# Optimization experiments

Measured on AMD Instinct MI355X. Metric: run time of the kernel, lower is better.

Reference implementation:

```python
import jax, jax.numpy as jnp
import numpy as np
from jax import lax

N = 200; E = 3200; HID = 64; NH = 16; OUT = 2 * HID; CAT = NH * OUT  # CAT = 2048
ALPHA = 0.2


def _gat(h, e_attr, adj, n2n, W, a_s, a_d, a_e, We, concat):
    # edge-feature-aware GAT head: logits from Wh_i, Wh_j and projected node2node feats
    Nn = h.shape[0]
    Wh = h @ W                                       # [N, out]
    ee = ((n2n @ We) @ a_e).reshape(Nn, Nn)          # [N, N] edge-feature term
    logits = jax.nn.leaky_relu((Wh @ a_s)[:, None] + (Wh @ a_d)[None, :] + ee,
                               negative_slope=ALPHA)
    logits = jnp.where(adj > 0, logits, -1e9)        # mask to graph structure
    att = jax.nn.softmax(logits, axis=1)
    h2 = att @ Wh
    if concat:
        h2 = jax.nn.elu(h2)
    return h2, jax.nn.elu(e_attr @ We)               # updated node + edge features


def _edge_pool(x, eidx, e, w, b):
    # static-shape edge pooling: score edges, gate nodes by mean incident score
    src, dst = eidx[0], eidx[1]
    s = jax.nn.sigmoid(jnp.concatenate([x[src], x[dst], e], axis=1) @ w + b)  # [E]
    deg = jax.ops.segment_sum(jnp.ones_like(s), src, num_segments=x.shape[0])
    ns = jax.ops.segment_sum(s, src, num_segments=x.shape[0]) / (deg + 1e-6)
    return x * ns[:, None], e * s[:, None]


def _gpool(x, w, b):
    # GlobalAttention: gate_nn = Linear+Sigmoid, softmax over nodes, weighted sum
    gate = jax.nn.softmax(jax.nn.sigmoid(x @ w + b), axis=0)  # [N, 1]
    return jnp.sum(gate * x, axis=0, keepdims=True)           # [1, D]


def _adj_n2n(Nn, eidx, eattr):
    # vectorized version of the per-edge Python loop in _get_adj_node2node
    src, dst = eidx[0], eidx[1]
    adj = jnp.zeros((Nn, Nn), eattr.dtype).at[src, dst].set(1.0)
    n2n = jnp.zeros((Nn * Nn, eattr.shape[1]), eattr.dtype).at[src * Nn + dst].set(eattr)
    return adj, n2n


def _lstm_dir(x, Wih, Whh, b):
    # one LSTM direction over seq x [T, Din] (PyTorch i,f,g,o gate order)
    Hh = Whh.shape[1]
    def step(carry, xt):
        h, c = carry
        g = xt @ Wih.T + h @ Whh.T + b
        i, f, gg, o = jnp.split(g, 4)
        c = jax.nn.sigmoid(f) * c + jax.nn.sigmoid(i) * jnp.tanh(gg)
        h = jax.nn.sigmoid(o) * jnp.tanh(c)
        return (h, c), h
    (_, _), ys = lax.scan(step, (jnp.zeros(Hh, x.dtype), jnp.zeros(Hh, x.dtype)), x)
    return ys


def setup_inputs():
    key = jax.random.key(0)
    ks = iter(jax.random.split(key, 64))
    def rn(shape, scale=0.05):
        return jax.random.normal(next(ks), shape, jnp.float32) * scale
    inp = {}
    for g in (1, 2):
        eidx = jax.random.randint(next(ks), (2, E), 0, N)
        eattr = rn((E, HID), 1.0)
        adj, n2n = _adj_n2n(N, eidx, eattr)
        inp['features%d' % g] = rn((N, HID), 1.0)
        inp['edge_index%d' % g] = eidx
        inp['edgesAttr%d' % g] = eattr
        inp['adjacency%d' % g] = adj
        inp['node2node%d' % g] = n2n
    inp.update(dict(
        W_h=rn((HID, HID)),
        W_gat=rn((NH, HID, OUT)), a_src=rn((NH, OUT)), a_dst=rn((NH, OUT)),
        a_e=rn((NH, OUT)), We_gat=rn((NH, HID, OUT)),
        W_out=rn((CAT, OUT)), ao_src=rn((OUT,)), ao_dst=rn((OUT,)), ao_e=rn((OUT,)),
        We_out=rn((CAT, OUT)),
        ep1_w=rn((3 * CAT,)), ep1_b=rn(()),
        ep2_w=rn((3 * OUT,)), ep2_b=rn(()),
        g1_w=rn((HID, 1)), g1_b=rn((1,)),
        g2_w=rn((CAT, 1)), g2_b=rn((1,)),
        g3_w=rn((OUT, 1)), g3_b=rn((1,)),
        Wih0=rn((2, 512, 35 * HID)), Whh0=rn((2, 512, 128)), b0=rn((2, 512)),
        Wih1=rn((2, 512, 256)), Whh1=rn((2, 512, 128)), b1=rn((2, 512)),
        fc_w=rn((256, 2)), fc_b=rn((2,)),
    ))
    return inp


def reference(features1, features2, edge_index1, edge_index2, edgesAttr1, edgesAttr2,
              adjacency1, adjacency2, node2node1, node2node2,
              W_h, W_gat, a_src, a_dst, a_e, We_gat,
              W_out, ao_src, ao_dst, ao_e, We_out,
              ep1_w, ep1_b, ep2_w, ep2_b,
              g1_w, g1_b, g2_w, g2_b, g3_w, g3_b,
              Wih0, Whh0, b0, Wih1, Whh1, b1, fc_w, fc_b):
    def graph(feat, eidx, eattr, adj, n2n):
        h = jax.nn.elu(feat @ W_h)                              # SingleNodeAttentionLayer
        hs = [_gpool(h, g1_w, g1_b)]
        outs = [_gat(h, eattr, adj, n2n, W_gat[i], a_src[i], a_dst[i], a_e[i],
                     We_gat[i], True) for i in range(NH)]
        h = jnp.concatenate([o[0] for o in outs], axis=1)       # [N, 2048]
        eattr = jnp.concatenate([o[1] for o in outs], axis=1)   # [E, 2048]
        h, eattr = _edge_pool(h, eidx, eattr, ep1_w, ep1_b)
        hs.append(_gpool(h, g2_w, g2_b))
        adj2, n2n2 = _adj_n2n(h.shape[0], eidx, eattr)          # dense [N*N, 2048]
        h, eattr = _gat(h, eattr, adj2, n2n2, W_out, ao_src, ao_dst, ao_e, We_out, False)
        h, eattr = _edge_pool(h, eidx, eattr, ep2_w, ep2_b)
        hs.append(_gpool(h, g3_w, g3_b))
        return jnp.concatenate(hs, axis=1)                      # [1, 35*HID]

    h1 = graph(features1, edge_index1, edgesAttr1, adjacency1, node2node1)
    h2 = graph(features2, edge_index2, edgesAttr2, adjacency2, node2node2)
    x = jnp.concatenate([h1, h2], axis=0)                       # seq [2, 2240]
    for Wih, Whh, b in ((Wih0, Whh0, b0), (Wih1, Whh1, b1)):
        f = _lstm_dir(x, Wih[0], Whh[0], b[0])
        r = _lstm_dir(x[::-1], Wih[1], Whh[1], b[1])[::-1]
        x = jnp.concatenate([f, r], axis=1)                     # [2, 256]
    logits = x[-1] @ fc_w + fc_b
    return jax.nn.softmax(logits)[None, :]                      # [1, nclass]
```

## Files before the change

kernel.cpp:

```cpp
#include <hip/hip_runtime.h>
#include <math.h>

#define DI static __device__ __forceinline__

DI float eluf(float x){ return x > 0.f ? x : expm1f(x); }
DI float lreluf(float x){ return x > 0.f ? x : 0.2f*x; }
DI float sigmf(float x){ return 1.f/(1.f+expf(-x)); }

typedef unsigned short u16;
typedef unsigned int   u32;
typedef __attribute__((ext_vector_type(8))) short short8_t;
typedef __attribute__((ext_vector_type(4))) float f32x4;

DI u16 bf16rne(float f){
  u32 u = __float_as_uint(f);
  u += 0x7fffu + ((u>>16)&1u);
  return (u16)(u>>16);
}

DI f32x4 bmfma(short8_t a, short8_t b, f32x4 c){
  return __builtin_amdgcn_mfma_f32_16x16x32_bf16(a, b, c, 0, 0, 0);
}

constexpr int N=200, E=3200, HID=64, NH=16, OUTD=128, CAT=2048, SEQD=2240;

constexpr int OH0   = 0;
constexpr int OWH   = OH0 + N*HID;
constexpr int OASN  = OWH + NH*N*OUTD;
constexpr int OADN  = OASN + NH*N;
constexpr int OH1   = OADN + NH*N;
constexpr int OXW1  = OH1 + N*CAT;
constexpr int OXW2  = OXW1 + 256;
constexpr int OEW1  = OXW2 + 256;
constexpr int OS1   = OEW1 + E;
constexpr int ODEG1 = OS1 + E;
constexpr int OSS1  = ODEG1 + 256;
constexpr int ORAW1 = OSS1 + 256;
constexpr int OWH2  = ORAW1 + 256;
constexpr int OAS2  = OWH2 + N*OUTD;
constexpr int OAD2  = OAS2 + 256;
constexpr int OEWV  = OAD2 + 256;
constexpr int OH2B  = OEWV + E;
constexpr int OXS2  = OH2B + N*OUTD;
constexpr int OXD2  = OXS2 + 256;
constexpr int ODEG2 = OXD2 + 256;
constexpr int OSS2  = ODEG2 + 256;
constexpr int ORAW2 = OSS2 + 256;
constexpr int ORAW3 = ORAW2 + 256;
constexpr int PGF   = ORAW3 + 256;
constexpr int GLOBF = 10624;
constexpr int TOTF  = GLOBF + 2*PGF;

__device__ __attribute__((aligned(16))) float G_F[TOTF];
__device__ float G_E2PART[(size_t)4*2*E*OUTD];
__device__ float G_EDOTH[2*NH*E];
__device__ float G_WHHT[2*2*128*512];
__device__ int   G_PIDX[2*N*N];
__device__ __attribute__((aligned(16))) u16 G_WGAT_T[NH*OUTD*HID];
__device__ __attribute__((aligned(16))) u16 G_WOUT_T[OUTD*CAT];
__device__ __attribute__((aligned(16))) u16 G_EATTR_BF[2*E*HID];

DI float* gf(int g){ return G_F + GLOBF + (size_t)g*PGF; }
DI float* gwe_ae(){ return G_F; }
DI float* gv_e(){ return G_F + 1024; }
DI float* gy0(){ return G_F + 3072; }
DI float* gy1(){ return G_F + 3584; }
DI float* gxseq(){ return G_F + 4096; }
DI float* gxg(){ return G_F + 8576; }
DI int*   gpidx(int g){ return G_PIDX + g*N*N; }

struct GraphIn {
  const float *feat, *eattr, *adj, *n2n;
  const int   *eidx;
};

struct Params {
  GraphIn g[2];
  const float *W_h, *W_gat, *a_src, *a_dst, *a_e, *We_gat;
  const float *W_out, *ao_src, *ao_dst, *ao_e, *We_out;
  const float *ep1_w, *ep1_b, *ep2_w, *ep2_b;
  const float *g1_w, *g1_b, *g2_w, *g2_b, *g3_w, *g3_b;
  const float *Wih0, *Whh0, *b0, *Wih1, *Whh1, *b1, *fc_w, *fc_b;
  float *out;
};

constexpr int ZPG  = 2*E + 1024;
constexpr int IB_Z = (2*ZPG+255)/256;
constexpr int IB_C = (2*N*N+255)/256;
constexpr int IB_D = 32;
constexpr int IB_E = (NH*HID+CAT+3)/4;
constexpr int IB_H = (2*N+3)/4;
constexpr int IB_W1 = 16;
constexpr int IB_W2 = 32;
constexpr int IB_EA = (2*E*HID)/256;
constexpr int IB_TOT = IB_Z+IB_C+IB_D+IB_E+IB_H+IB_W1+IB_W2+IB_EA;
__global__ __launch_bounds__(256) void k_init(Params P){
  __shared__ __attribute__((aligned(16))) float ldt[8320];
  int b = blockIdx.x, tid = threadIdx.x;
  if (b < IB_Z){
    int i = b*256 + tid;
    if (i < 2*ZPG){
      int g = i/ZPG, r = i%ZPG;
      int addr = r<E ? OEW1+r : (r<2*E ? OEWV+(r-E) :
                 (r<2*E+512 ? ODEG1+(r-2*E) : ODEG2+(r-2*E-512)));
      gf(g)[addr] = 0.f;
    }
  } else if (b < IB_Z+IB_C){
    int i = (b-IB_Z)*256 + tid; if (i < 2*N*N) G_PIDX[i] = -1;
  } else if (b < IB_Z+IB_C+IB_D){
    int tt = b-(IB_Z+IB_C);
    int ld = tt>>3, gt0 = (tt&7)*64;
    int l = ld>>1, d = ld&1;
    const float* Whh = l ? P.Whh1 : P.Whh0;
    const float* src = Whh + ((size_t)d*512 + gt0)*128;
    #pragma unroll
    for (int i=0;i<32;i++){
      int idx = tid + i*256;
      int gl = idx>>7, k = idx&127;
      ldt[gl*129 + k] = src[idx];
    }
    __syncthreads();
    float* dst = G_WHHT + (size_t)ld*128*512 + gt0;
    #pragma unroll
    for (int i=0;i<32;i++){
      int idx = tid + i*256;
      int gl = idx&63, k = idx>>6;
      dst[(size_t)k*512 + gl] = ldt[gl*129 + k];
    }
  } else if (b < IB_Z+IB_C+IB_D+IB_E){
    int gid = (b-IB_Z-IB_C-IB_D)*4 + (tid>>6);
    int lane = tid & 63;
    if (gid < NH*HID){
      int h = gid/HID, c = gid%HID;
      const float* W = P.We_gat + (size_t)(h*HID+c)*OUTD;
      const float* a = P.a_e + h*OUTD;
      float acc = 0.f;
      for (int o=lane;o<OUTD;o+=64) acc += W[o]*a[o];
      for (int off=32;off>0;off>>=1) acc += __shfl_down(acc,off);
      if (lane==0) gwe_ae()[gid] = acc;
    } else if (gid < NH*HID+CAT){
      int c = gid - NH*HID;
      const float* W = P.We_out + (size_t)c*OUTD;
      float acc = 0.f;
      for (int o=lane;o<OUTD;o+=64) acc += W[o]*P.ao_e[o];
      for (int off=32;off>0;off>>=1) acc += __shfl_down(acc,off);
      if (lane==0) gv_e()[c] = acc;
    }
  } else if (b < IB_Z+IB_C+IB_D+IB_E+IB_H){
    int unit = (b-IB_Z-IB_C-IB_D-IB_E)*4 + (tid>>6);
    if (unit >= 2*N) return;
    int g = unit / N, n = unit % N, c = tid & 63;
    const float* feat = P.g[g].feat;
    float acc = 0.f;
    for (int k=0;k<HID;k++) acc += feat[n*HID+k]*P.W_h[k*HID+c];
    float v = eluf(acc);
    float* f = gf(g);
    f[OH0 + n*HID + c] = v;
    float r = v*P.g1_w[c];
    for (int off=32;off>0;off>>=1) r += __shfl_down(r,off);
    if (c==0) f[ORAW1+n] = r;
  } else if (b < IB_Z+IB_C+IB_D+IB_E+IB_H+IB_W1){
    int h = b-(IB_Z+IB_C+IB_D+IB_E+IB_H);
    const float* src = P.We_gat + (size_t)h*HID*OUTD;
    #pragma unroll
    for (int i=0;i<32;i++){
      int idx = tid + i*256;
      int c = idx>>7, o = idx&127;
      ldt[o*65 + c] = src[idx];
    }
    __syncthreads();
    u16* dst = G_WGAT_T + (size_t)h*OUTD*HID;
    #pragma unroll
    for (int i=0;i<32;i++){
      int idx = tid + i*256;
      int c = idx&63, o = idx>>6;
      dst[o*64 + c] = bf16rne(ldt[o*65 + c]);
    }
  } else if (b < IB_Z+IB_C+IB_D+IB_E+IB_H+IB_W1+IB_W2){
    int tt = b-(IB_Z+IB_C+IB_D+IB_E+IB_H+IB_W1);
    int q0 = (tt>>1)*128, n0 = (tt&1)*64;
    #pragma unroll
    for (int i=0;i<32;i++){
      int idx = tid + i*256;
      int nl = idx&63, ql = idx>>6;
      ldt[ql*65 + nl] = P.We_out[(size_t)(q0+ql)*OUTD + n0 + nl];
    }
    __syncthreads();
    #pragma unroll
    for (int i=0;i<32;i++){
      int idx = tid + i*256;
      int ql = idx&127, nl = idx>>7;
      G_WOUT_T[(size_t)(n0+nl)*CAT + q0 + ql] = bf16rne(ldt[ql*65 + nl]);
    }
  } else {
    int i = (b-(IB_Z+IB_C+IB_D+IB_E+IB_H+IB_W1+IB_W2))*256 + tid;
    int g = i >= E*HID ? 1 : 0;
    G_EATTR_BF[i] = bf16rne(P.g[g].eattr[i - g*E*HID]);
  }
}


DI void e2p_body(Params& P, int idx, char* smem){
  int g = idx/400, r2 = idx%400, hg = r2/100, eb = r2%100;
  int tid = threadIdx.x;
  int wave = tid>>6, lane = tid&63, l16 = lane&15, l4 = lane>>4;
  u16* Tlds = (u16*)smem;
  int e0 = eb*32;
  int nt0 = wave*2;
  const u16* ea = G_EATTR_BF + ((size_t)g*E + e0)*HID;
  short8_t af00 = *(const short8_t*)(ea + l16*HID + l4*8);
  short8_t af01 = *(const short8_t*)(ea + l16*HID + 32 + l4*8);
  short8_t af10 = *(const short8_t*)(ea + (16+l16)*HID + l4*8);
  short8_t af11 = *(const short8_t*)(ea + (16+l16)*HID + 32 + l4*8);
  float ew1p0[4] = {0.f,0.f,0.f,0.f}, ewvp0[4] = {0.f,0.f,0.f,0.f};
  float ew1p1[4] = {0.f,0.f,0.f,0.f}, ewvp1[4] = {0.f,0.f,0.f,0.f};
  for (int hh=0; hh<4; hh++){
    int h = hg*4 + hh;
    const u16* Wg = G_WGAT_T + (size_t)h*OUTD*HID;
    #pragma unroll
    for (int nn=0; nn<2; nn++){
      int nt = nt0 + nn;
      const u16* Wgn = Wg + (size_t)(nt*16 + l16)*HID + l4*8;
      short8_t wg0 = *(const short8_t*)Wgn;
      short8_t wg1 = *(const short8_t*)(Wgn + 32);
      f32x4 d0 = {0.f,0.f,0.f,0.f}, d1 = {0.f,0.f,0.f,0.f};
      d0 = bmfma(af00, wg0, d0);
      d1 = bmfma(af10, wg0, d1);
      d0 = bmfma(af01, wg1, d0);
      d1 = bmfma(af11, wg1, d1);
      int qg = h*OUTD + nt*16 + l16;
      float w1 = P.ep1_w[2*CAT + qg];
      float wv = gv_e()[qg];
      int qloc = hh*128 + nt*16 + l16;
      #pragma unroll
      for (int r=0;r<4;r++){
        float v0 = d0[r] > 0.f ? d0[r] : expm1f(d0[r]);
        float v1 = d1[r] > 0.f ? d1[r] : expm1f(d1[r]);
        ew1p0[r] += v0*w1; ewvp0[r] += v0*wv;
        ew1p1[r] += v1*w1; ewvp1[r] += v1*wv;
        int row = l4*4 + r;
        int byt = (row*1024 + qloc*2) ^ ((row&7)<<4);
        *(u16*)((char*)Tlds + byt) = bf16rne(v0);
        *(u16*)((char*)Tlds + byt + 16384) = bf16rne(v1);
      }
    }
  }
  const u16* WoA = G_WOUT_T + (size_t)(wave*32 + l16)*CAT + hg*512 + l4*8;
  const u16* WoB = WoA + 16*CAT;
  short8_t w0a = *(const short8_t*)WoA;
  short8_t w0b = *(const short8_t*)WoB;
  short8_t w1a = *(const short8_t*)(WoA + 32);
  short8_t w1b = *(const short8_t*)(WoB + 32);
  float* f = gf(g);
  #pragma unroll
  for (int r=0;r<4;r++){
    float a0 = ew1p0[r], b0 = ewvp0[r], a1 = ew1p1[r], b1 = ewvp1[r];
    a0 += __shfl_xor(a0,1); b0 += __shfl_xor(b0,1); a1 += __shfl_xor(a1,1); b1 += __shfl_xor(b1,1);
    a0 += __shfl_xor(a0,2); b0 += __shfl_xor(b0,2); a1 += __shfl_xor(a1,2); b1 += __shfl_xor(b1,2);
    a0 += __shfl_xor(a0,4); b0 += __shfl_xor(b0,4); a1 += __shfl_xor(a1,4); b1 += __shfl_xor(b1,4);
    a0 += __shfl_xor(a0,8); b0 += __shfl_xor(b0,8); a1 += __shfl_xor(a1,8); b1 += __shfl_xor(b1,8);
    if (l16==0){
      int e = e0 + l4*4 + r;
      atomicAdd(&f[OEW1+e], a0);
      atomicAdd(&f[OEWV+e], b0);
      atomicAdd(&f[OEW1+e+16], a1);
      atomicAdd(&f[OEWV+e+16], b1);
    }
  }
  __syncthreads();
  f32x4 acc00 = {0.f,0.f,0.f,0.f}, acc01 = {0.f,0.f,0.f,0.f};
  f32x4 acc10 = {0.f,0.f,0.f,0.f}, acc11 = {0.f,0.f,0.f,0.f};
  #pragma unroll
  for (int ks=0; ks<16; ks++){
    short8_t na = w0a, nb = w0b;
    if (ks < 14){
      na = *(const short8_t*)(WoA + (ks+2)*32);
      nb = *(const short8_t*)(WoB + (ks+2)*32);
    }
    int byt = (l16*1024 + ks*64 + l4*16) ^ ((l16&7)<<4);
    short8_t a0 = *(const short8_t*)((const char*)Tlds + byt);
    short8_t a1 = *(const short8_t*)((const char*)Tlds + byt + 16384);
    acc00 = bmfma(a0, w0a, acc00);
    acc10 = bmfma(a1, w0a, acc10);
    acc01 = bmfma(a0, w0b, acc01);
    acc11 = bmfma(a1, w0b, acc11);
    w0a = w1a; w0b = w1b; w1a = na; w1b = nb;
  }
  float* dst = G_E2PART + (((size_t)hg*2 + g)*E + e0)*OUTD;
  #pragma unroll
  for (int r=0;r<4;r++){
    int ee = l4*4 + r;
    dst[(size_t)ee*OUTD + wave*32 + l16]      = acc00[r];
    dst[(size_t)ee*OUTD + wave*32 + 16 + l16] = acc01[r];
    dst[(size_t)(16+ee)*OUTD + wave*32 + l16]      = acc10[r];
    dst[(size_t)(16+ee)*OUTD + wave*32 + 16 + l16] = acc11[r];
  }
}

DI void edoth_body(Params& P, int idx, float* s){
  int tid = threadIdx.x;
  int g = idx / (E/16);
  int e0 = (idx % (E/16)) * 16;
  float (*ea)[HID+1] = (float(*)[HID+1])s;
  float (*wa)[HID+1] = (float(*)[HID+1])(s + 16*(HID+1));
  {
    int row = tid >> 4, c0 = (tid & 15)*4;
    float4 v = *(const float4*)&P.g[g].eattr[(size_t)(e0+row)*HID + c0];
    ea[row][c0]=v.x; ea[row][c0+1]=v.y; ea[row][c0+2]=v.z; ea[row][c0+3]=v.w;
    float4 w = *(const float4*)&gwe_ae()[row*HID + c0];
    wa[row][c0]=w.x; wa[row][c0+1]=w.y; wa[row][c0+2]=w.z; wa[row][c0+3]=w.w;
  }
  __syncthreads();
  int h = tid >> 4, el = tid & 15;
  float acc = 0.f;
  #pragma unroll
  for (int c=0;c<HID;c++) acc += ea[el][c]*wa[h][c];
  G_EDOTH[((size_t)g*NH + h)*E + e0 + el] = acc;
}

DI void wh_body(Params& P, int idx, float* s){
  int o = threadIdx.x;
  if (o >= 128) return;
  int g = idx / (N*(NH+1));
  int r = idx % (N*(NH+1));
  int h = r / N, n = r % N;
  float* f = gf(g);
  if (h == NH){
    if (n != 0) return;
    float* att = s;
    float* sb  = s + 200;
    for (int j = o; j < N; j += 128) att[j] = sigmf(f[ORAW1+j] + P.g1_b[0]);
    __syncthreads();
    float m = -3e38f;
    for (int j = o; j < N; j += 128) m = fmaxf(m, att[j]);
    sb[o] = m; __syncthreads();
    for (int sft=64;sft>0;sft>>=1){ if (o<sft) sb[o]=fmaxf(sb[o],sb[o+sft]); __syncthreads(); }
    m = sb[0]; __syncthreads();
    float ss = 0.f;
    for (int j = o; j < N; j += 128){ float e = expf(att[j]-m); ss += e; }
    sb[o] = ss; __syncthreads();
    for (int sft=64;sft>0;sft>>=1){ if (o<sft) sb[o]+=sb[o+sft]; __syncthreads(); }
    float inv = 1.f/sb[0]; __syncthreads();
    for (int j = o; j < N; j += 128) att[j] = expf(att[j]-m)*inv;
    __syncthreads();
    if (o < HID){
      float acc = 0.f;
      for (int j=0;j<N;j++) acc += att[j]*f[OH0 + j*HID + o];
      gxseq()[g*SEQD + o] = acc;
    }
    return;
  }
  float* hs   = s;
  float* sred = s + 64;
  float* dred = s + 192;
  if (o < HID) hs[o] = f[OH0 + n*HID + o];
  __syncthreads();
  const float* W = P.W_gat + (size_t)h*HID*OUTD + o;
  float acc = 0.f;
  for (int c=0;c<HID;c++) acc += hs[c]*W[(size_t)c*OUTD];
  f[OWH + ((size_t)h*N + n)*OUTD + o] = acc;
  sred[o] = acc*P.a_src[h*OUTD+o];
  dred[o] = acc*P.a_dst[h*OUTD+o];
  __syncthreads();
  for (int sft=64;sft>0;sft>>=1){ if (o<sft){ sred[o]+=sred[o+sft]; dred[o]+=dred[o+sft]; } __syncthreads(); }
  if (o==0){ f[OASN+h*N+n]=sred[0]; f[OADN+h*N+n]=dred[0]; }
}

DI void pairs_body(Params& P, int idx){
  int g = idx / 13;
  int e = (idx % 13)*256 + threadIdx.x;
  if (e >= E) return;
  const int* ei = P.g[g].eidx;
  atomicMax(&gpidx(g)[ei[e]*N + ei[E+e]], e);
}

constexpr int MB_E2P = 800, MB_ED = 400, MB_WH = 2*N*(NH+1), MB_PR = 26;
__global__ __launch_bounds__(256) void k_mega(Params P){
  __shared__ __attribute__((aligned(16))) char smem[32768];
  int b = blockIdx.x;
  if (b < MB_E2P) e2p_body(P, b, smem);
  else if (b < MB_E2P+MB_ED) edoth_body(P, b-MB_E2P, (float*)smem);
  else if (b < MB_E2P+MB_ED+MB_WH) wh_body(P, b-(MB_E2P+MB_ED), (float*)smem);
  else pairs_body(P, b-(MB_E2P+MB_ED+MB_WH));
}

__global__ void k_att1(Params P){
  int nb = blockIdx.x, h = blockIdx.y, g = blockIdx.z, tid = threadIdx.x;
  int n0 = nb*4;
  __shared__ float z[4][N];
  __shared__ float red[128];
  __shared__ float sinv[4];
  float* f = gf(g);
  const float* adj = P.g[g].adj;
  const int* pidx = gpidx(g);
  const float* edoth = G_EDOTH + ((size_t)g*NH + h)*E;
  const float* adn = f + OADN + h*N;
  for (int i=0;i<4;i++){
    float asn = f[OASN + h*N + n0+i];
    for (int j = tid; j < N; j += 128){
      float a = adj[(n0+i)*N + j];
      float zz;
      if (a > 0.f){
        int p = pidx[(n0+i)*N + j];
        float ee = (p >= 0) ? edoth[p] : 0.f;
        zz = lreluf(asn + adn[j] + ee);
      } else zz = -1e9f;
      z[i][j] = zz;
    }
  }
  __syncthreads();
  for (int i=0;i<4;i++){
    float m = -3e38f;
    for (int j = tid; j < N; j += 128) m = fmaxf(m, z[i][j]);
    red[tid] = m; __syncthreads();
    for (int s=64;s>0;s>>=1){ if (tid<s) red[tid]=fmaxf(red[tid],red[tid+s]); __syncthreads(); }
    m = red[0]; __syncthreads();
    float ssum = 0.f;
    for (int j = tid; j < N; j += 128){ float e = expf(z[i][j]-m); z[i][j]=e; ssum += e; }
    red[tid] = ssum; __syncthreads();
    for (int s=64;s>0;s>>=1){ if (tid<s) red[tid]+=red[tid+s]; __syncthreads(); }
    if (tid==0) sinv[i] = 1.f/red[0];
    __syncthreads();
  }
  const float* wh = f + OWH + (size_t)h*N*OUTD;
  float a0=0.f,a1=0.f,a2=0.f,a3=0.f;
  for (int j=0;j<N;j++){
    float w = wh[(size_t)j*OUTD + tid];
    a0 += z[0][j]*w; a1 += z[1][j]*w; a2 += z[2][j]*w; a3 += z[3][j]*w;
  }
  f[OH1 + (size_t)(n0+0)*CAT + h*OUTD + tid] = eluf(a0*sinv[0]);
  f[OH1 + (size_t)(n0+1)*CAT + h*OUTD + tid] = eluf(a1*sinv[1]);
  f[OH1 + (size_t)(n0+2)*CAT + h*OUTD + tid] = eluf(a2*sinv[2]);
  f[OH1 + (size_t)(n0+3)*CAT + h*OUTD + tid] = eluf(a3*sinv[3]);
}

__global__ void k_xw1(Params P){
  int n = blockIdx.x, g = blockIdx.y, tid = threadIdx.x;
  __shared__ float s1b[256], s2b[256], s3b[256];
  float* f = gf(g);
  const float* x = f + OH1 + (size_t)n*CAT;
  float a1 = 0.f, a2 = 0.f, a3 = 0.f;
  for (int c = tid; c < CAT; c += 256){
    float xv = x[c];
    a1 += xv*P.ep1_w[c];
    a2 += xv*P.ep1_w[CAT+c];
    a3 += xv*P.g2_w[c];
  }
  s1b[tid]=a1; s2b[tid]=a2; s3b[tid]=a3; __syncthreads();
  for (int s=128;s>0;s>>=1){
    if (tid<s){ s1b[tid]+=s1b[tid+s]; s2b[tid]+=s2b[tid+s]; s3b[tid]+=s3b[tid+s]; }
    __syncthreads();
  }
  if (tid==0){ f[OXW1+n]=s1b[0]; f[OXW2+n]=s2b[0]; f[ORAW2+n]=s3b[0]; }
}

__global__ void k_s1(Params P){
  int e = blockIdx.x*256 + threadIdx.x, g = blockIdx.y;
  if (e >= E) return;
  float* f = gf(g);
  const int* ei = P.g[g].eidx;
  int s = ei[e], d = ei[E+e];
  float v = sigmf(f[OXW1+s] + f[OXW2+d] + f[OEW1+e] + P.ep1_b[0]);
  f[OS1+e] = v;
  atomicAdd(&f[OSS1+s], v);
  atomicAdd(&f[ODEG1+s], 1.f);
}

DI void gpool_body(Params& P, int xoff, int D, int odeg, int rawoff,
                   const float* bb, int outoff, int cb, int g,
                   float* att, float* sb){
  int tid = threadIdx.x;
  float* f = gf(g);
  if (tid < N){
    float sc = f[odeg+256+tid]/(f[odeg+tid]+1e-6f);
    att[tid] = sigmf(f[rawoff+tid]*sc + bb[0]);
  }
  __syncthreads();
  float m = (tid < N) ? att[tid] : -3e38f;
  sb[tid] = m; __syncthreads();
  for (int s=256;s>0;s>>=1){ if (tid<s) sb[tid]=fmaxf(sb[tid],sb[tid+s]); __syncthreads(); }
  m = sb[0]; __syncthreads();
  float e = (tid < N) ? expf(att[tid]-m) : 0.f;
  sb[tid] = e; __syncthreads();
  for (int s=256;s>0;s>>=1){ if (tid<s) sb[tid]+=sb[tid+s]; __syncthreads(); }
  float inv = 1.f/sb[0]; __syncthreads();
  if (tid < N){
    float sc = f[odeg+256+tid]/(f[odeg+tid]+1e-6f);
    att[tid] = e*inv*sc;
  }
  __syncthreads();
  int c = cb*512 + tid;
  if (c < D){
    const float* x = f + xoff;
    float acc = 0.f;
    for (int n=0;n<N;n++) acc += att[n]*x[(size_t)n*D + c];
    gxseq()[g*SEQD + outoff + c] = acc;
  }
}

__global__ __launch_bounds__(512) void k_pool2(Params P){
  __shared__ float att[256];
  __shared__ float sb[512];
  int b = blockIdx.x;
  int g = b >> 2, cb = b & 3;
  gpool_body(P, OH1, CAT, ODEG1, ORAW2, P.g2_b, HID, cb, g, att, sb);
}

__global__ __launch_bounds__(512) void k_pool3(Params P){
  __shared__ float att[256];
  __shared__ float sb[512];
  int g = blockIdx.x;
  gpool_body(P, OH2B, OUTD, ODEG2, ORAW3, P.g3_b, HID+CAT, 0, g, att, sb);
}

__global__ void k_Wh2(Params P){
  int n = blockIdx.x, g = blockIdx.y, tid = threadIdx.x;
  int kq = tid >> 7, o = tid & 127;
  __shared__ float hrow[4][128];
  __shared__ float part[4][128];
  __shared__ float sr[128], dr[128];
  float* f = gf(g);
  const float* x = f + OH1 + (size_t)n*CAT;
  float acc = 0.f;
  for (int cc=0; cc<4; cc++){
    int c0 = kq*512 + cc*128;
    __syncthreads();
    hrow[kq][o] = x[c0 + o];
    __syncthreads();
    const float* W = P.W_out + (size_t)c0*OUTD + o;
    for (int j=0;j<128;j++) acc += hrow[kq][j]*W[(size_t)j*OUTD];
  }
  part[kq][o] = acc;
  __syncthreads();
  if (kq==0){
    float ns = f[OSS1+n]/(f[ODEG1+n]+1e-6f);
    float a = part[0][o]+part[1][o]+part[2][o]+part[3][o];
    float v = a*ns;
    f[OWH2 + (size_t)n*OUTD + o] = v;
    sr[o] = v*P.ao_src[o];
    dr[o] = v*P.ao_dst[o];
  }
  __syncthreads();
  for (int s=64;s>0;s>>=1){
    if (tid<s){ sr[tid]+=sr[tid+s]; dr[tid]+=dr[tid+s]; }
    __syncthreads();
  }
  if (tid==0){ f[OAS2+n]=sr[0]; f[OAD2+n]=dr[0]; }
}

__global__ void k_att2(Params P){
  int n = blockIdx.x, g = blockIdx.y, tid = threadIdx.x;
  __shared__ float z[N];
  __shared__ float red[128];
  __shared__ float dred[128];
  __shared__ float gred[128];
  float* f = gf(g);
  const float* adj = P.g[g].adj;
  const int* pidx = gpidx(g);
  float asn = f[OAS2+n];
  const float* adn = f + OAD2;
  for (int j = tid; j < N; j += 128){
    float a = adj[n*N + j];
    float zz;
    if (a > 0.f){
      int p = pidx[n*N + j];
      float ee = (p >= 0) ? f[OEWV+p]*f[OS1+p] : 0.f;
      zz = lreluf(asn + adn[j] + ee);
    } else zz = -1e9f;
    z[j] = zz;
  }
  __syncthreads();
  float m = -3e38f;
  for (int j = tid; j < N; j += 128) m = fmaxf(m, z[j]);
  red[tid] = m; __syncthreads();
  for (int s=64;s>0;s>>=1){ if (tid<s) red[tid]=fmaxf(red[tid],red[tid+s]); __syncthreads(); }
  m = red[0]; __syncthreads();
  float ssum = 0.f;
  for (int j = tid; j < N; j += 128){ float e = expf(z[j]-m); z[j]=e; ssum += e; }
  red[tid] = ssum; __syncthreads();
  for (int s=64;s>0;s>>=1){ if (tid<s) red[tid]+=red[tid+s]; __syncthreads(); }
  float inv = 1.f/red[0]; __syncthreads();
  const float* wh = f + OWH2;
  float acc = 0.f;
  for (int j=0;j<N;j++){
    float w = z[j];
    if (w != 0.f) acc += w * wh[(size_t)j*OUTD + tid];
  }
  float v = acc*inv;
  f[OH2B + (size_t)n*OUTD + tid] = v;
  red[tid]  = v*P.ep2_w[tid];
  dred[tid] = v*P.ep2_w[OUTD+tid];
  gred[tid] = v*P.g3_w[tid];
  __syncthreads();
  for (int s=64;s>0;s>>=1){
    if (tid<s){ red[tid]+=red[tid+s]; dred[tid]+=dred[tid+s]; gred[tid]+=gred[tid+s]; }
    __syncthreads();
  }
  if (tid==0){ f[OXS2+n]=red[0]; f[OXD2+n]=dred[0]; f[ORAW3+n]=gred[0]; }
}

constexpr int TE2 = 16;
__global__ void k_ew2fin(Params P){
  int e0 = blockIdx.x*TE2, g = blockIdx.y, tid = threadIdx.x;
  __shared__ float lred[2][TE2];
  float* f = gf(g);
  float w2 = P.ep2_w[2*OUTD + tid];
  int lane = tid & 63, wvi = tid >> 6;
  for (int e=0;e<TE2;e++){
    const float* src = G_E2PART + ((size_t)g*E + e0 + e)*OUTD + tid;
    float a = 0.f;
    #pragma unroll
    for (int h=0;h<4;h++) a += src[(size_t)h*2*E*OUTD];
    float v = eluf(f[OS1+e0+e]*a) * w2;
    for (int off=32;off>0;off>>=1) v += __shfl_down(v,off);
    if (lane==0) lred[wvi][e]=v;
  }
  __syncthreads();
  if (tid < TE2){
    int e = e0 + tid;
    float ew2 = lred[0][tid]+lred[1][tid];
    const int* ei = P.g[g].eidx;
    int s = ei[e], d = ei[E+e];
    float v = sigmf(f[OXS2+s] + f[OXD2+d] + ew2 + P.ep2_b[0]);
    atomicAdd(&f[OSS2+s], v);
    atomicAdd(&f[ODEG2+s], 1.f);
  }
}

__global__ void k_lstm_xg(Params P, int layer){
  int gid = blockIdx.x*4 + (threadIdx.x>>6);
  int lane = threadIdx.x & 63;
  int t = gid >> 10;
  int rem = gid & 1023;
  int d = rem >> 9;
  int gate = rem & 511;
  const float* Wih = layer ? P.Wih1 : P.Wih0;
  const float* bb  = layer ? P.b1   : P.b0;
  const float* xin = layer ? gy0()  : gxseq();
  int Din = layer ? 256 : SEQD;
  const float* x = xin + t*Din;
  const float* Wr = Wih + ((size_t)d*512 + gate)*Din;
  float acc = 0.f;
  for (int k=lane; k<Din; k+=64) acc += x[k]*Wr[k];
  for (int off=32; off>0; off>>=1) acc += __shfl_down(acc, off);
  if (lane==0) gxg()[(t*2 + d)*512 + gate] = acc + bb[d*512 + gate];
}

__global__ void k_lstm_rec(Params P, int layer){
  int d = blockIdx.x, tid = threadIdx.x;
  float* yout = layer ? gy1() : gy0();
  const float* T = G_WHHT + (size_t)(layer*2 + d)*128*512;
  __shared__ float h[128], c[128], gbuf[512];
  if (tid < 128){ h[tid]=0.f; c[tid]=0.f; }
  __syncthreads();
  for (int s=0;s<2;s++){
    int t = (d==0) ? s : 1-s;
    float acc = gxg()[(t*2 + d)*512 + tid];
    for (int k=0;k<128;k++) acc += h[k]*T[(size_t)k*512 + tid];
    gbuf[tid] = acc;
    __syncthreads();
    if (tid < 128){
      float ii = sigmf(gbuf[tid]);
      float ff = sigmf(gbuf[128+tid]);
      float gg = tanhf(gbuf[256+tid]);
      float oo = sigmf(gbuf[384+tid]);
      float cn = ff*c[tid] + ii*gg;
      c[tid] = cn;
      float hn = oo*tanhf(cn);
      h[tid] = hn;
      yout[t*256 + d*128 + tid] = hn;
    }
    __syncthreads();
  }
}

__global__ __launch_bounds__(1024) void k_recfin(Params P){
  int tid = threadIdx.x;
  int d = tid>>9, gt = tid&511;
  __shared__ float h[2][128], c[2][128], gbuf[2][512], yfin[256];
  __shared__ float sb[256], sb2[256];
  if (gt < 128){ h[d][gt]=0.f; c[d][gt]=0.f; }
  __syncthreads();
  const float* T = G_WHHT + (size_t)(2 + d)*128*512;
  for (int s=0;s<2;s++){
    int t = (d==0) ? s : 1-s;
    float acc = gxg()[(t*2 + d)*512 + gt];
    for (int k=0;k<128;k++) acc += h[d][k]*T[(size_t)k*512 + gt];
    gbuf[d][gt] = acc;
    __syncthreads();
    if (gt < 128){
      float ii = sigmf(gbuf[d][gt]);
      float ff = sigmf(gbuf[d][128+gt]);
      float gg = tanhf(gbuf[d][256+gt]);
      float oo = sigmf(gbuf[d][384+gt]);
      float cn = ff*c[d][gt] + ii*gg;
      c[d][gt] = cn;
      float hn = oo*tanhf(cn);
      h[d][gt] = hn;
      if (t==1) yfin[d*128 + gt] = hn;
    }
    __syncthreads();
  }
  if (tid < 256){
    sb[tid]  = yfin[tid]*P.fc_w[tid*2+0];
    sb2[tid] = yfin[tid]*P.fc_w[tid*2+1];
  }
  __syncthreads();
  for (int s=128;s>0;s>>=1){
    if (tid<s){ sb[tid]+=sb[tid+s]; sb2[tid]+=sb2[tid+s]; }
    __syncthreads();
  }
  if (tid==0){
    float l0 = sb[0] + P.fc_b[0];
    float l1 = sb2[0] + P.fc_b[1];
    float m = fmaxf(l0,l1);
    float e0 = expf(l0-m), e1 = expf(l1-m), inv = 1.f/(e0+e1);
    P.out[0] = e0*inv;
    P.out[1] = e1*inv;
  }
}

extern "C" void kernel_launch(void* const* d_in, const int* in_sizes, int n_in,
                              void* d_out, int out_size, void* d_ws, size_t ws_size,
                              hipStream_t stream){
  Params P;
  for (int g=0; g<2; ++g){
    int b = g*5;
    P.g[g].feat  = (const float*)d_in[b+0];
    P.g[g].eidx  = (const int*)d_in[b+1];
    P.g[g].eattr = (const float*)d_in[b+2];
    P.g[g].adj   = (const float*)d_in[b+3];
    P.g[g].n2n   = (const float*)d_in[b+4];
  }
  P.W_h   = (const float*)d_in[10];
  P.W_gat = (const float*)d_in[11];
  P.a_src = (const float*)d_in[12];
  P.a_dst = (const float*)d_in[13];
  P.a_e   = (const float*)d_in[14];
  P.We_gat= (const float*)d_in[15];
  P.W_out = (const float*)d_in[16];
  P.ao_src= (const float*)d_in[17];
  P.ao_dst= (const float*)d_in[18];
  P.ao_e  = (const float*)d_in[19];
  P.We_out= (const float*)d_in[20];
  P.ep1_w = (const float*)d_in[21];
  P.ep1_b = (const float*)d_in[22];
  P.ep2_w = (const float*)d_in[23];
  P.ep2_b = (const float*)d_in[24];
  P.g1_w  = (const float*)d_in[25];
  P.g1_b  = (const float*)d_in[26];
  P.g2_w  = (const float*)d_in[27];
  P.g2_b  = (const float*)d_in[28];
  P.g3_w  = (const float*)d_in[29];
  P.g3_b  = (const float*)d_in[30];
  P.Wih0  = (const float*)d_in[31];
  P.Whh0  = (const float*)d_in[32];
  P.b0    = (const float*)d_in[33];
  P.Wih1  = (const float*)d_in[34];
  P.Whh1  = (const float*)d_in[35];
  P.b1    = (const float*)d_in[36];
  P.fc_w  = (const float*)d_in[37];
  P.fc_b  = (const float*)d_in[38];
  P.out   = (float*)d_out;

  k_init <<<dim3(IB_TOT), 256, 0, stream>>>(P);
  k_mega <<<dim3(MB_E2P+MB_ED+MB_WH+MB_PR), 256, 0, stream>>>(P);
  k_att1 <<<dim3(N/4,NH,2),128, 0, stream>>>(P);
  k_xw1  <<<dim3(N,2),    256, 0, stream>>>(P);
  k_s1   <<<dim3((E+255)/256,2), 256, 0, stream>>>(P);
  k_pool2<<<dim3(8),      512, 0, stream>>>(P);
  k_Wh2  <<<dim3(N,2),    512, 0, stream>>>(P);
  k_att2 <<<dim3(N,2),    128, 0, stream>>>(P);
  k_ew2fin<<<dim3(E/TE2,2),128, 0, stream>>>(P);
  k_pool3<<<dim3(2),      512, 0, stream>>>(P);
  k_lstm_xg <<<dim3(512), 256, 0, stream>>>(P, 0);
  k_lstm_rec<<<dim3(2),   512, 0, stream>>>(P, 0);
  k_lstm_xg <<<dim3(512), 256, 0, stream>>>(P, 1);
  k_recfin<<<dim3(1),    1024, 0, stream>>>(P);
}
```

Before: 359.7 us.

## Compute second GAT projection with bf16 MFMA using bf16 copy of layer-1 output

k_att1 now also writes a bf16 copy of the layer-1 node features. The per-node scalar FP32 GEMV kernel for Wh2 (h1 @ W_out) is replaced by a 16-row-tiled MFMA kernel that reads that copy and the pre-transposed bf16 W_out. Attention source and destination dot products are reduced with wave shuffles and atomics, so their buffers are now zeroed in k_init. The aim is to cut the FP32 FMA cost and the repeated W_out reads, at the price of bf16 rounding, extra stores in k_att1, and only 26 blocks of parallelism.

```diff
diff --git a/kernel.cpp b/kernel.cpp
--- a/kernel.cpp
+++ b/kernel.cpp
@@ -59,6 +59,7 @@
 __device__ __attribute__((aligned(16))) u16 G_WGAT_T[NH*OUTD*HID];
 __device__ __attribute__((aligned(16))) u16 G_WOUT_T[OUTD*CAT];
 __device__ __attribute__((aligned(16))) u16 G_EATTR_BF[2*E*HID];
+__device__ __attribute__((aligned(16))) u16 G_H1BF[2*N*CAT];
 
 DI float* gf(int g){ return G_F + GLOBF + (size_t)g*PGF; }
 DI float* gwe_ae(){ return G_F; }
@@ -84,7 +85,7 @@
   float *out;
 };
 
-constexpr int ZPG  = 2*E + 1024;
+constexpr int ZPG  = 2*E + 1024 + 512;
 constexpr int IB_Z = (2*ZPG+255)/256;
 constexpr int IB_C = (2*N*N+255)/256;
 constexpr int IB_D = 32;
@@ -101,8 +102,13 @@
     int i = b*256 + tid;
     if (i < 2*ZPG){
       int g = i/ZPG, r = i%ZPG;
-      int addr = r<E ? OEW1+r : (r<2*E ? OEWV+(r-E) :
-                 (r<2*E+512 ? ODEG1+(r-2*E) : ODEG2+(r-2*E-512)));
+      int addr;
+      if (r < E) addr = OEW1+r;
+      else if (r < 2*E) addr = OEWV+(r-E);
+      else if (r < 2*E+512) addr = ODEG1+(r-2*E);
+      else if (r < 2*E+1024) addr = ODEG2+(r-2*E-512);
+      else if (r < 2*E+1280) addr = OAS2+(r-2*E-1024);
+      else addr = OAD2+(r-2*E-1280);
       gf(g)[addr] = 0.f;
     }
   } else if (b < IB_Z+IB_C){
@@ -428,10 +434,19 @@
     float w = wh[(size_t)j*OUTD + tid];
     a0 += z[0][j]*w; a1 += z[1][j]*w; a2 += z[2][j]*w; a3 += z[3][j]*w;
   }
-  f[OH1 + (size_t)(n0+0)*CAT + h*OUTD + tid] = eluf(a0*sinv[0]);
-  f[OH1 + (size_t)(n0+1)*CAT + h*OUTD + tid] = eluf(a1*sinv[1]);
-  f[OH1 + (size_t)(n0+2)*CAT + h*OUTD + tid] = eluf(a2*sinv[2]);
-  f[OH1 + (size_t)(n0+3)*CAT + h*OUTD + tid] = eluf(a3*sinv[3]);
+  float v0 = eluf(a0*sinv[0]);
+  float v1 = eluf(a1*sinv[1]);
+  float v2 = eluf(a2*sinv[2]);
+  float v3 = eluf(a3*sinv[3]);
+  f[OH1 + (size_t)(n0+0)*CAT + h*OUTD + tid] = v0;
+  f[OH1 + (size_t)(n0+1)*CAT + h*OUTD + tid] = v1;
+  f[OH1 + (size_t)(n0+2)*CAT + h*OUTD + tid] = v2;
+  f[OH1 + (size_t)(n0+3)*CAT + h*OUTD + tid] = v3;
+  u16* hb = G_H1BF + ((size_t)g*N + n0)*CAT + h*OUTD + tid;
+  hb[0*CAT] = bf16rne(v0);
+  hb[1*CAT] = bf16rne(v1);
+  hb[2*CAT] = bf16rne(v2);
+  hb[3*CAT] = bf16rne(v3);
 }
 
 __global__ void k_xw1(Params P){
@@ -513,39 +528,48 @@
   gpool_body(P, OH2B, OUTD, ODEG2, ORAW3, P.g3_b, HID+CAT, 0, g, att, sb);
 }
 
-__global__ void k_Wh2(Params P){
-  int n = blockIdx.x, g = blockIdx.y, tid = threadIdx.x;
-  int kq = tid >> 7, o = tid & 127;
-  __shared__ float hrow[4][128];
-  __shared__ float part[4][128];
-  __shared__ float sr[128], dr[128];
+__global__ __launch_bounds__(256) void k_wh2m(Params P){
+  int mt = blockIdx.x, g = blockIdx.y;
+  int tid = threadIdx.x;
+  int wave = tid>>6, lane = tid&63, l16 = lane&15, l4 = lane>>4;
+  int n0 = mt*16;
   float* f = gf(g);
-  const float* x = f + OH1 + (size_t)n*CAT;
-  float acc = 0.f;
-  for (int cc=0; cc<4; cc++){
-    int c0 = kq*512 + cc*128;
-    __syncthreads();
-    hrow[kq][o] = x[c0 + o];
-    __syncthreads();
-    const float* W = P.W_out + (size_t)c0*OUTD + o;
-    for (int j=0;j<128;j++) acc += hrow[kq][j]*W[(size_t)j*OUTD];
-  }
-  part[kq][o] = acc;
-  __syncthreads();
-  if (kq==0){
-    float ns = f[OSS1+n]/(f[ODEG1+n]+1e-6f);
-    float a = part[0][o]+part[1][o]+part[2][o]+part[3][o];
-    float v = a*ns;
-    f[OWH2 + (size_t)n*OUTD + o] = v;
-    sr[o] = v*P.ao_src[o];
-    dr[o] = v*P.ao_dst[o];
-  }
-  __syncthreads();
-  for (int s=64;s>0;s>>=1){
-    if (tid<s){ sr[tid]+=sr[tid+s]; dr[tid]+=dr[tid+s]; }
-    __syncthreads();
-  }
-  if (tid==0){ f[OAS2+n]=sr[0]; f[OAD2+n]=dr[0]; }
+  int arow_n = n0 + l16;
+  bool av = arow_n < N;
+  const u16* arow = G_H1BF + ((size_t)g*N + (av ? arow_n : 0))*CAT + l4*8;
+  const u16* bp0 = G_WOUT_T + (size_t)(wave*32 + l16)*CAT + l4*8;
+  const u16* bp1 = bp0 + (size_t)16*CAT;
+  short8_t az = {0,0,0,0,0,0,0,0};
+  f32x4 acc0 = {0.f,0.f,0.f,0.f}, acc1 = {0.f,0.f,0.f,0.f};
+  #pragma unroll 8
+  for (int ks=0; ks<64; ks++){
+    short8_t a = av ? *(const short8_t*)(arow + ks*32) : az;
+    short8_t b0 = *(const short8_t*)(bp0 + ks*32);
+    short8_t b1 = *(const short8_t*)(bp1 + ks*32);
+    acc0 = bmfma(a, b0, acc0);
+    acc1 = bmfma(a, b1, acc1);
+  }
+  #pragma unroll
+  for (int r=0;r<4;r++){
+    int node = n0 + l4*4 + r;
+    if (node < N){
+      float ns = f[OSS1+node]/(f[ODEG1+node]+1e-6f);
+      float v0 = acc0[r]*ns, v1 = acc1[r]*ns;
+      int c0 = wave*32 + l16, c1 = c0 + 16;
+      f[OWH2 + (size_t)node*OUTD + c0] = v0;
+      f[OWH2 + (size_t)node*OUTD + c1] = v1;
+      float ps = v0*P.ao_src[c0] + v1*P.ao_src[c1];
+      float pd = v0*P.ao_dst[c0] + v1*P.ao_dst[c1];
+      ps += __shfl_xor(ps,1); pd += __shfl_xor(pd,1);
+      ps += __shfl_xor(ps,2); pd += __shfl_xor(pd,2);
+      ps += __shfl_xor(ps,4); pd += __shfl_xor(pd,4);
+      ps += __shfl_xor(ps,8); pd += __shfl_xor(pd,8);
+      if (l16==0){
+        atomicAdd(&f[OAS2+node], ps);
+        atomicAdd(&f[OAD2+node], pd);
+      }
+    }
+  }
 }
 
 __global__ void k_att2(Params P){
@@ -769,7 +793,7 @@
   k_xw1  <<<dim3(N,2),    256, 0, stream>>>(P);
   k_s1   <<<dim3((E+255)/256,2), 256, 0, stream>>>(P);
   k_pool2<<<dim3(8),      512, 0, stream>>>(P);
-  k_Wh2  <<<dim3(N,2),    512, 0, stream>>>(P);
+  k_wh2m <<<dim3(13,2),   256, 0, stream>>>(P);
   k_att2 <<<dim3(N,2),    128, 0, stream>>>(P);
   k_ew2fin<<<dim3(E/TE2,2),128, 0, stream>>>(P);
   k_pool3<<<dim3(2),      512, 0, stream>>>(P);
```

After: 361.8 us. No clear change (+0.6%).

## Regroup mega-kernels so att1 runs alongside e2p, and fuse pool2 into Wh2

Applied to the files above, without the earlier changes.

Splits the first mega-kernel in two. Edge-dot, Wh and pair-index work run first. The edge-to-pair work then shares a launch with the layer-1 attention blocks, which are now a device function driven by a flat block index. Separately, the gated pooling for layer 2 is merged into the Wh2 kernel as extra blocks. The aim is to remove a launch and fill the GPU with independent work so tail blocks overlap. The risks are 256-thread blocks where half the threads exit early before barriers in att1, and reduced shared memory in the first mega kernel.

```diff
diff --git a/kernel.cpp b/kernel.cpp
--- a/kernel.cpp
+++ b/kernel.cpp
@@ -374,22 +374,16 @@
   atomicMax(&gpidx(g)[ei[e]*N + ei[E+e]], e);
 }
 
-constexpr int MB_E2P = 800, MB_ED = 400, MB_WH = 2*N*(NH+1), MB_PR = 26;
-__global__ __launch_bounds__(256) void k_mega(Params P){
-  __shared__ __attribute__((aligned(16))) char smem[32768];
-  int b = blockIdx.x;
-  if (b < MB_E2P) e2p_body(P, b, smem);
-  else if (b < MB_E2P+MB_ED) edoth_body(P, b-MB_E2P, (float*)smem);
-  else if (b < MB_E2P+MB_ED+MB_WH) wh_body(P, b-(MB_E2P+MB_ED), (float*)smem);
-  else pairs_body(P, b-(MB_E2P+MB_ED+MB_WH));
-}
-
-__global__ void k_att1(Params P){
-  int nb = blockIdx.x, h = blockIdx.y, g = blockIdx.z, tid = threadIdx.x;
+DI void att1_body(Params& P, int idx, float* s){
+  int tid = threadIdx.x;
+  if (tid >= 128) return;
+  int g = idx / 800;
+  int r2 = idx % 800;
+  int h = r2 / 50, nb = r2 % 50;
   int n0 = nb*4;
-  __shared__ float z[4][N];
-  __shared__ float red[128];
-  __shared__ float sinv[4];
+  float (*z)[N] = (float(*)[N])s;
+  float* red  = s + 800;
+  float* sinv = s + 928;
   float* f = gf(g);
   const float* adj = P.g[g].adj;
   const int* pidx = gpidx(g);
@@ -413,12 +407,12 @@
     float m = -3e38f;
     for (int j = tid; j < N; j += 128) m = fmaxf(m, z[i][j]);
     red[tid] = m; __syncthreads();
-    for (int s=64;s>0;s>>=1){ if (tid<s) red[tid]=fmaxf(red[tid],red[tid+s]); __syncthreads(); }
+    for (int ss=64;ss>0;ss>>=1){ if (tid<ss) red[tid]=fmaxf(red[tid],red[tid+ss]); __syncthreads(); }
     m = red[0]; __syncthreads();
     float ssum = 0.f;
     for (int j = tid; j < N; j += 128){ float e = expf(z[i][j]-m); z[i][j]=e; ssum += e; }
     red[tid] = ssum; __syncthreads();
-    for (int s=64;s>0;s>>=1){ if (tid<s) red[tid]+=red[tid+s]; __syncthreads(); }
+    for (int ss=64;ss>0;ss>>=1){ if (tid<ss) red[tid]+=red[tid+ss]; __syncthreads(); }
     if (tid==0) sinv[i] = 1.f/red[0];
     __syncthreads();
   }
@@ -432,6 +426,23 @@
   f[OH1 + (size_t)(n0+1)*CAT + h*OUTD + tid] = eluf(a1*sinv[1]);
   f[OH1 + (size_t)(n0+2)*CAT + h*OUTD + tid] = eluf(a2*sinv[2]);
   f[OH1 + (size_t)(n0+3)*CAT + h*OUTD + tid] = eluf(a3*sinv[3]);
+}
+
+constexpr int MA_ED = 400, MA_WH = 2*N*(NH+1), MA_PR = 26;
+__global__ __launch_bounds__(256) void k_mega_a(Params P){
+  __shared__ __attribute__((aligned(16))) float smem[2080];
+  int b = blockIdx.x;
+  if (b < MA_ED) edoth_body(P, b, smem);
+  else if (b < MA_ED+MA_WH) wh_body(P, b-MA_ED, smem);
+  else pairs_body(P, b-(MA_ED+MA_WH));
+}
+
+constexpr int MB_E2P = 800, MB_A1 = 1600;
+__global__ __launch_bounds__(256) void k_mega_b(Params P){
+  __shared__ __attribute__((aligned(16))) char smem[32768];
+  int b = blockIdx.x;
+  if (b < MB_E2P) e2p_body(P, b, smem);
+  else att1_body(P, b-MB_E2P, (float*)smem);
 }
 
 __global__ void k_xw1(Params P){
@@ -498,27 +509,12 @@
   }
 }
 
-__global__ __launch_bounds__(512) void k_pool2(Params P){
-  __shared__ float att[256];
-  __shared__ float sb[512];
-  int b = blockIdx.x;
-  int g = b >> 2, cb = b & 3;
-  gpool_body(P, OH1, CAT, ODEG1, ORAW2, P.g2_b, HID, cb, g, att, sb);
-}
-
-__global__ __launch_bounds__(512) void k_pool3(Params P){
-  __shared__ float att[256];
-  __shared__ float sb[512];
-  int g = blockIdx.x;
-  gpool_body(P, OH2B, OUTD, ODEG2, ORAW3, P.g3_b, HID+CAT, 0, g, att, sb);
-}
-
-__global__ void k_Wh2(Params P){
-  int n = blockIdx.x, g = blockIdx.y, tid = threadIdx.x;
+DI void wh2_body(Params& P, int n, int g, float* hrow4, float* part4,
+                 float* sr, float* dr){
+  int tid = threadIdx.x;
   int kq = tid >> 7, o = tid & 127;
-  __shared__ float hrow[4][128];
-  __shared__ float part[4][128];
-  __shared__ float sr[128], dr[128];
+  float (*hrow)[128] = (float(*)[128])hrow4;
+  float (*part)[128] = (float(*)[128])part4;
   float* f = gf(g);
   const float* x = f + OH1 + (size_t)n*CAT;
   float acc = 0.f;
@@ -546,6 +542,24 @@
     __syncthreads();
   }
   if (tid==0){ f[OAS2+n]=sr[0]; f[OAD2+n]=dr[0]; }
+}
+
+__global__ __launch_bounds__(512) void k_wh2p2(Params P){
+  __shared__ float sa[512], sbb[512], sc2[128], sd[128];
+  int b = blockIdx.x;
+  if (b < 400){
+    wh2_body(P, b>>1, b&1, sa, sbb, sc2, sd);
+  } else {
+    int idx = b-400, g = idx>>2, cb = idx&3;
+    gpool_body(P, OH1, CAT, ODEG1, ORAW2, P.g2_b, HID, cb, g, sa, sbb);
+  }
+}
+
+__global__ __launch_bounds__(512) void k_pool3(Params P){
+  __shared__ float att[256];
+  __shared__ float sb[512];
+  int g = blockIdx.x;
+  gpool_body(P, OH2B, OUTD, ODEG2, ORAW3, P.g3_b, HID+CAT, 0, g, att, sb);
 }
 
 __global__ void k_att2(Params P){
@@ -763,18 +777,17 @@
   P.fc_b  = (const float*)d_in[38];
   P.out   = (float*)d_out;
 
-  k_init <<<dim3(IB_TOT), 256, 0, stream>>>(P);
-  k_mega <<<dim3(MB_E2P+MB_ED+MB_WH+MB_PR), 256, 0, stream>>>(P);
-  k_att1 <<<dim3(N/4,NH,2),128, 0, stream>>>(P);
-  k_xw1  <<<dim3(N,2),    256, 0, stream>>>(P);
-  k_s1   <<<dim3((E+255)/256,2), 256, 0, stream>>>(P);
-  k_pool2<<<dim3(8),      512, 0, stream>>>(P);
-  k_Wh2  <<<dim3(N,2),    512, 0, stream>>>(P);
-  k_att2 <<<dim3(N,2),    128, 0, stream>>>(P);
+  k_init  <<<dim3(IB_TOT), 256, 0, stream>>>(P);
+  k_mega_a<<<dim3(MA_ED+MA_WH+MA_PR), 256, 0, stream>>>(P);
+  k_mega_b<<<dim3(MB_E2P+MB_A1), 256, 0, stream>>>(P);
+  k_xw1   <<<dim3(N,2),    256, 0, stream>>>(P);
+  k_s1    <<<dim3((E+255)/256,2), 256, 0, stream>>>(P);
+  k_wh2p2 <<<dim3(408),    512, 0, stream>>>(P);
+  k_att2  <<<dim3(N,2),    128, 0, stream>>>(P);
   k_ew2fin<<<dim3(E/TE2,2),128, 0, stream>>>(P);
-  k_pool3<<<dim3(2),      512, 0, stream>>>(P);
-  k_lstm_xg <<<dim3(512), 256, 0, stream>>>(P, 0);
-  k_lstm_rec<<<dim3(2),   512, 0, stream>>>(P, 0);
-  k_lstm_xg <<<dim3(512), 256, 0, stream>>>(P, 1);
-  k_recfin<<<dim3(1),    1024, 0, stream>>>(P);
-}
+  k_pool3 <<<dim3(2),      512, 0, stream>>>(P);
+  k_lstm_xg <<<dim3(512),  256, 0, stream>>>(P, 0);
+  k_lstm_rec<<<dim3(2),    512, 0, stream>>>(P, 0);
+  k_lstm_xg <<<dim3(512),  256, 0, stream>>>(P, 1);
+  k_recfin<<<dim3(1),     1024, 0, stream>>>(P);
+}
```

Result: faster. 351.3 us (-2.4%).
